# Performance work log

Hardware: AMD Instinct MI355X
Metric: run time of the kernel (lower is better)

The kernel has to match this reference:

```python
import jax, jax.numpy as jnp
import numpy as np

B = 4096            # batch size
NQ, NL = 4, 2       # qubits, variational layers
H = W = 28          # image size -> 14x14 patches of 2x2
NP = (H // 2) * (W // 2)  # 196 patches per image


def setup_inputs() -> dict:
    key = jax.random.key(0)
    k1, k2, k3, k4 = jax.random.split(key, 4)
    x = jax.random.randint(k1, (B, 1, H, W), 0, 256, dtype=jnp.int32)
    params = jax.random.normal(k2, (NQ, NL), dtype=jnp.float32)
    fc_w = jax.random.normal(k3, (10, NQ * NP), dtype=jnp.float32) * 0.02
    fc_b = jax.random.normal(k4, (10,), dtype=jnp.float32) * 0.02
    return {"x": x, "params": params, "fc_w": fc_w, "fc_b": fc_b}


def _cnot(state, c):
    # state: (N, 2,2,2,2); CNOT with control qubit c, target c+1
    s0 = state[(slice(None),) * (c + 1) + (0,)]          # control=0 branch
    s1 = state[(slice(None),) * (c + 1) + (1,)]          # control=1 branch
    # after removing control axis c+1, the target axis (was c+2) is c+1
    return jnp.stack([s0, jnp.flip(s1, axis=c + 1)], axis=c + 1)


def _forward(x, params, fc_w, fc_b):
    # angle encoding: pi * pixel / 255
    ang = jnp.pi * (x.astype(jnp.float32) / 255.0)       # (B,1,28,28)
    ang = ang[:, 0]                                      # (B,28,28)
    # 2x2 patches, row-major over (r,c), patch flattened row-major -> 4 angles
    th = ang.reshape(B, H // 2, 2, W // 2, 2).transpose(0, 1, 3, 2, 4)
    th = th.reshape(B * NP, NQ)                          # (N, 4)

    # RY(theta) on |0> gives [cos(t/2), sin(t/2)] per qubit -> product state
    v = jnp.stack([jnp.cos(th * 0.5), jnp.sin(th * 0.5)], axis=-1)  # (N,4,2)
    state = jnp.einsum('na,nb,nc,nd->nabcd', v[:, 0], v[:, 1], v[:, 2], v[:, 3])
    state = state.astype(jnp.complex64)                  # (N,2,2,2,2)

    for l in range(NL):
        for w in range(NQ):
            phi = params[w, l]
            # RZ(phi) = diag(e^{-i phi/2}, e^{+i phi/2}) on qubit w
            ph = jnp.stack([jnp.exp(-0.5j * phi), jnp.exp(0.5j * phi)])
            shape = [1] * 5
            shape[w + 1] = 2
            state = state * ph.reshape(shape)
        for w in range(NQ - 1):
            state = _cnot(state, w)

    probs = state.real ** 2 + state.imag ** 2            # (N,2,2,2,2)
    zs = []
    for i in range(NQ):
        other = tuple(a for a in range(1, 5) if a != i + 1)
        m = jnp.sum(probs, axis=other)                   # (N,2)
        zs.append(m[:, 0] - m[:, 1])                     # <Z_i>
    meas = jnp.stack(zs, axis=-1)                        # (N,4)

    features = meas.reshape(B, NP * NQ)                  # patch-major, 4 per patch
    logits = features @ fc_w.T + fc_b
    return jax.nn.log_softmax(logits, axis=-1)


def reference(x, params, fc_w, fc_b):
    return _forward(x, params, fc_w, fc_b)
```

## Files before the change

### kernel.cpp

```cpp
#include <hip/hip_runtime.h>
#include <math.h>

#define BD 256
#define IPB 4
#define NPIX 784
#define NOUT 10

__global__ __launch_bounds__(BD) void quanv_analytic_kernel(
    const int* __restrict__ x,
    const float* __restrict__ fc_w,
    const float* __restrict__ fc_b,
    float* __restrict__ out,
    int B)
{
    __shared__ int   img[IPB * NPIX];
    __shared__ float lut[256];

    const int t  = threadIdx.x;
    const int b0 = blockIdx.x * IPB;

    lut[t] = cosf((float)t * (3.14159265358979323846f / 255.0f));

    {
        const int4* src = (const int4*)(x + (size_t)b0 * NPIX);
        int4* dst = (int4*)img;
        const int nvec = IPB * NPIX / 4;
        for (int k = t; k < nvec; k += BD) {
            if (b0 * NPIX / 4 + k < (B * NPIX) / 4) dst[k] = src[k];
        }
    }
    __syncthreads();

    const int wv   = t >> 6;
    const int lane = t & 63;
    const int b    = b0 + wv;
    if (b >= B) return;
    const int* im = img + wv * NPIX;

    float acc[NOUT];
#pragma unroll
    for (int o = 0; o < NOUT; ++o) acc[o] = 0.0f;

    for (int f = lane; f < NPIX; f += 64) {
        const int p = f >> 2, c = f & 3;
        const int i = p / 14, j = p - i * 14;
        const int base = i * 56 + j * 2 + (c & 1);
        float fv = lut[im[base]];
        fv *= (c & 2) ? lut[im[base + 28]] : 1.0f;
#pragma unroll
        for (int o = 0; o < NOUT; ++o) acc[o] += fv * fc_w[o * NPIX + f];
    }

#pragma unroll
    for (int o = 0; o < NOUT; ++o) {
#pragma unroll
        for (int off = 32; off > 0; off >>= 1)
            acc[o] += __shfl_xor(acc[o], off, 64);
    }

    if (lane == 0) {
        float lg[NOUT];
        float m = -1e30f;
#pragma unroll
        for (int o = 0; o < NOUT; ++o) {
            lg[o] = acc[o] + fc_b[o];
            m = fmaxf(m, lg[o]);
        }
        float sum = 0.0f;
#pragma unroll
        for (int o = 0; o < NOUT; ++o) sum += expf(lg[o] - m);
        const float lse = m + logf(sum);
        float* ob = out + (size_t)b * NOUT;
#pragma unroll
        for (int o = 0; o < NOUT; ++o) ob[o] = lg[o] - lse;
    }
}

extern "C" void kernel_launch(void* const* d_in, const int* in_sizes, int n_in,
                              void* d_out, int out_size, void* d_ws, size_t ws_size,
                              hipStream_t stream) {
    const int*   x      = (const int*)d_in[0];
    const float* fc_w   = (const float*)d_in[2];
    const float* fc_b   = (const float*)d_in[3];
    float* out = (float*)d_out;
    const int B = in_sizes[0] / NPIX;
    const int grid = (B + IPB - 1) / IPB;
    quanv_analytic_kernel<<<grid, BD, 0, stream>>>(x, fc_w, fc_b, out, B);
}
```

Measured before the change: 15.37 us.

## Drop LDS staging and LUT; map lanes to patches with vector loads

Each wave now reads its image directly from global memory with int2 loads instead of staging images through LDS behind a barrier. Cosines come from the hardware cos builtin (argument in revolutions, v/510) rather than a shared lookup table. Each lane handles a whole patch and reads the four FC weights per output as one float4. Blocks shrink to two waves, which gives more, smaller blocks, but every lane now issues uncoalesced strided global loads and the hardware cosine may be less precise.

```diff
diff --git a/kernel.cpp b/kernel.cpp
--- a/kernel.cpp
+++ b/kernel.cpp
@@ -1,54 +1,53 @@
 #include <hip/hip_runtime.h>
 #include <math.h>
 
-#define BD 256
-#define IPB 4
+#define BD 128
+#define IPB 2
 #define NPIX 784
 #define NOUT 10
 
-__global__ __launch_bounds__(BD) void quanv_analytic_kernel(
+__device__ __forceinline__ float cospix(int v) {
+    return __builtin_amdgcn_cosf((float)v * (1.0f / 510.0f));
+}
+
+__global__ __launch_bounds__(BD) void quanv_analytic2_kernel(
     const int* __restrict__ x,
     const float* __restrict__ fc_w,
     const float* __restrict__ fc_b,
     float* __restrict__ out,
     int B)
 {
-    __shared__ int   img[IPB * NPIX];
-    __shared__ float lut[256];
-
-    const int t  = threadIdx.x;
-    const int b0 = blockIdx.x * IPB;
-
-    lut[t] = cosf((float)t * (3.14159265358979323846f / 255.0f));
-
-    {
-        const int4* src = (const int4*)(x + (size_t)b0 * NPIX);
-        int4* dst = (int4*)img;
-        const int nvec = IPB * NPIX / 4;
-        for (int k = t; k < nvec; k += BD) {
-            if (b0 * NPIX / 4 + k < (B * NPIX) / 4) dst[k] = src[k];
-        }
-    }
-    __syncthreads();
-
+    const int t    = threadIdx.x;
     const int wv   = t >> 6;
     const int lane = t & 63;
-    const int b    = b0 + wv;
+    const int b    = blockIdx.x * IPB + wv;
     if (b >= B) return;
-    const int* im = img + wv * NPIX;
+
+    const int* im = x + (size_t)b * NPIX;
 
     float acc[NOUT];
 #pragma unroll
     for (int o = 0; o < NOUT; ++o) acc[o] = 0.0f;
 
-    for (int f = lane; f < NPIX; f += 64) {
-        const int p = f >> 2, c = f & 3;
-        const int i = p / 14, j = p - i * 14;
-        const int base = i * 56 + j * 2 + (c & 1);
-        float fv = lut[im[base]];
-        fv *= (c & 2) ? lut[im[base + 28]] : 1.0f;
 #pragma unroll
-        for (int o = 0; o < NOUT; ++o) acc[o] += fv * fc_w[o * NPIX + f];
+    for (int k = 0; k < 4; ++k) {
+        const int p = lane + 64 * k;
+        if (p < 196) {
+            const int i = p / 14;
+            const int j = p - i * 14;
+            const int base = i * 56 + j * 2;
+            const int2 top = *(const int2*)(im + base);
+            const int2 bot = *(const int2*)(im + base + 28);
+            const float A = cospix(top.x);
+            const float Bv = cospix(top.y);
+            const float f2 = A * cospix(bot.x);
+            const float f3 = Bv * cospix(bot.y);
+#pragma unroll
+            for (int o = 0; o < NOUT; ++o) {
+                const float4 w = *(const float4*)(fc_w + o * NPIX + 4 * p);
+                acc[o] += A * w.x + Bv * w.y + f2 * w.z + f3 * w.w;
+            }
+        }
     }
 
 #pragma unroll
@@ -85,5 +84,5 @@
     float* out = (float*)d_out;
     const int B = in_sizes[0] / NPIX;
     const int grid = (B + IPB - 1) / IPB;
-    quanv_analytic_kernel<<<grid, BD, 0, stream>>>(x, fc_w, fc_b, out, B);
+    quanv_analytic2_kernel<<<grid, BD, 0, stream>>>(x, fc_w, fc_b, out, B);
 }
```

New measurement: 14.49 us. 5.7% less time.
